# Kernel tuning notes

Measured on AMD Instinct MI355X. Metric: run time of the kernel, lower is better.

Reference implementation:

```python
import jax, jax.numpy as jnp
import numpy as np

EMBED_DIM = 1024
HEAD_SIZE = 128
B, S = 8, 2048

def setup_inputs() -> dict:
    rng = jax.random.key(0)
    k1, k2, k3, k4, k5, k6 = jax.random.split(rng, 6)
    std = 1.0 / EMBED_DIM  # nn.initializers.normal(stddev=1/embed_dim)
    return {
        "key": jax.random.normal(k1, (B, S, EMBED_DIM), dtype=jnp.float32),
        "query": jax.random.normal(k2, (B, S, EMBED_DIM), dtype=jnp.float32),
        "value": jax.random.normal(k3, (B, S, EMBED_DIM), dtype=jnp.float32),
        "W_Q": jax.random.normal(k4, (EMBED_DIM, HEAD_SIZE), dtype=jnp.float32) * std,
        "W_K": jax.random.normal(k5, (EMBED_DIM, HEAD_SIZE), dtype=jnp.float32) * std,
        "W_V": jax.random.normal(k6, (EMBED_DIM, HEAD_SIZE), dtype=jnp.float32) * std,
    }

def reference(key, query, value, W_Q, W_K, W_V):
    # Parallel retention: (Q K^T * causal_mask) V
    q_proj = query @ W_Q        # (B, S, H)
    k_proj = key @ W_K          # (B, S, H)
    v_proj = value @ W_V        # (B, S, H)
    ret = jnp.einsum("bsh,bth->bst", q_proj, k_proj)  # (B, S, S)
    # full_self_retention=False -> lower-triangular (causal) mask
    decay_matrix = jnp.tril(jnp.ones((S, S), dtype=ret.dtype))
    ret = ret * decay_matrix
    return ret @ v_proj          # (B, S, H)
```

## Files before the change

### kernel.cpp

```cpp
#include <hip/hip_runtime.h>
#include <cstdint>

#define B_  8
#define S_  2048
#define E_  1024
#define H_  128
#define NC_ 16

typedef __attribute__((ext_vector_type(8))) short bf16x8;
typedef __attribute__((ext_vector_type(4))) float f32x4;

__device__ __forceinline__ short f2bf(float f){
  uint32_t u = __builtin_bit_cast(uint32_t, f);
  u = (u + 0x7fffu + ((u >> 16) & 1u)) >> 16;
  return (short)u;
}
__device__ __forceinline__ float bf2f(short s){
  uint32_t u = ((uint32_t)(uint16_t)s) << 16;
  return __builtin_bit_cast(float, u);
}

__global__ __launch_bounds__(256) void wt_kernel(
    const float* __restrict__ WQ, const float* __restrict__ WK,
    const float* __restrict__ WV,
    short* __restrict__ WtQ, short* __restrict__ WtK, short* __restrict__ WtV)
{
  int which = blockIdx.z;
  const float* W = which == 0 ? WQ : which == 1 ? WK : WV;
  short* Wt      = which == 0 ? WtQ : which == 1 ? WtK : WtV;
  int k0 = blockIdx.x * 32, n0 = blockIdx.y * 32;
  __shared__ float t[32][33];
  int tx = threadIdx.x & 31, ty = threadIdx.x >> 5;
  #pragma unroll
  for (int i = 0; i < 4; i++)
    t[ty + i * 8][tx] = W[(size_t)(k0 + ty + i * 8) * H_ + n0 + tx];
  __syncthreads();
  #pragma unroll
  for (int i = 0; i < 4; i++)
    Wt[(size_t)(n0 + ty + i * 8) * E_ + k0 + tx] = f2bf(t[tx][ty + i * 8]);
}

__global__ __launch_bounds__(256) void proj_kernel(
    const float* __restrict__ Xq, const float* __restrict__ Xk,
    const float* __restrict__ Xv,
    const short* __restrict__ Wtq, const short* __restrict__ Wtk,
    const short* __restrict__ Wtv,
    short* __restrict__ q, short* __restrict__ k,
    short* __restrict__ kT, short* __restrict__ vT)
{
  int which = blockIdx.y;
  const float* X  = which == 0 ? Xq  : which == 1 ? Xk  : Xv;
  const short* Wt = which == 0 ? Wtq : which == 1 ? Wtk : Wtv;

  int tid = threadIdx.x, lane = tid & 63, wave = tid >> 6;
  int lr = lane & 15, lq = lane >> 4;
  int rowbase = blockIdx.x * 64 + wave * 16;

  __shared__ short Bs[128 * 136];

  const float* xr = X + (size_t)(rowbase + lr) * E_ + lq * 8;

  f32x4 acc[8];
  #pragma unroll
  for (int tn = 0; tn < 8; tn++) acc[tn] = (f32x4){0.f, 0.f, 0.f, 0.f};

  for (int kc = 0; kc < 8; kc++){
    if (kc) __syncthreads();
    #pragma unroll
    for (int v = 0; v < 8; v++){
      int c = v * 256 + tid;
      int n = c >> 4, off = (c & 15) * 8;
      *(bf16x8*)(&Bs[n * 136 + off]) =
          *(const bf16x8*)(Wt + (size_t)n * E_ + kc * 128 + off);
    }
    f32x4 ar[8];
    #pragma unroll
    for (int s = 0; s < 4; s++){
      ar[2 * s]     = *(const f32x4*)(xr + kc * 128 + s * 32);
      ar[2 * s + 1] = *(const f32x4*)(xr + kc * 128 + s * 32 + 4);
    }
    __syncthreads();
    #pragma unroll
    for (int s = 0; s < 4; s++){
      bf16x8 a;
      #pragma unroll
      for (int j = 0; j < 4; j++){
        a[j] = f2bf(ar[2 * s][j]); a[4 + j] = f2bf(ar[2 * s + 1][j]);
      }
      #pragma unroll
      for (int tn = 0; tn < 8; tn++){
        bf16x8 bfr = *(const bf16x8*)(&Bs[(tn * 16 + lr) * 136 + s * 32 + lq * 8]);
        acc[tn] = __builtin_amdgcn_mfma_f32_16x16x32_bf16(a, bfr, acc[tn], 0, 0, 0);
      }
    }
  }

  if (which <= 1){
    short* P = which == 0 ? q : k;
    #pragma unroll
    for (int tn = 0; tn < 8; tn++)
      #pragma unroll
      for (int r4 = 0; r4 < 4; r4++)
        P[(size_t)(rowbase + lq * 4 + r4) * H_ + tn * 16 + lr] = f2bf(acc[tn][r4]);
  }
  if (which >= 1){
    short* T = which == 1 ? kT : vT;
    int b = rowbase >> 11, srow = rowbase & 2047;
    #pragma unroll
    for (int tn = 0; tn < 8; tn++){
      union { short sh[4]; uint2 u; } pk;
      #pragma unroll
      for (int r4 = 0; r4 < 4; r4++) pk.sh[r4] = f2bf(acc[tn][r4]);
      *(uint2*)(T + ((size_t)b * H_ + tn * 16 + lr) * S_ + srow + lq * 4) = pk.u;
    }
  }
}

__global__ __launch_bounds__(256) void fused_state(
    const short* __restrict__ vT, const short* __restrict__ kT,
    short* __restrict__ Shi, short* __restrict__ Slo)
{
  int rh = blockIdx.x;
  int ch = blockIdx.y;
  int b  = blockIdx.z;
  int tid = threadIdx.x, lane = tid & 63, wave = tid >> 6;
  int lr = lane & 15, lq = lane >> 4;

  __shared__ short As[2][32 * 136];
  __shared__ short Bs[2][64 * 136];

  const short* vtb = vT + (size_t)b * H_ * S_ + (size_t)(rh * 32) * S_;
  const short* ktb = kT + (size_t)b * H_ * S_ + (size_t)(ch * 64) * S_;

  f32x4 acc[2];
  acc[0] = (f32x4){0.f, 0.f, 0.f, 0.f};
  acc[1] = (f32x4){0.f, 0.f, 0.f, 0.f};

  for (int j = 0; j < NC_; j++){
    size_t obase = (size_t)(b * NC_ + j) * 16384;
    #pragma unroll
    for (int tm = 0; tm < 2; tm++)
      #pragma unroll
      for (int r4 = 0; r4 < 4; r4++){
        int row = rh * 32 + tm * 16 + lq * 4 + r4;
        int col = ch * 64 + wave * 16 + lr;
        float v = acc[tm][r4];
        short h = f2bf(v);
        Shi[obase + (size_t)row * 128 + col] = h;
        Slo[obase + (size_t)row * 128 + col] = f2bf(v - bf2f(h));
      }
    if (j == NC_ - 1) break;

    int buf = j & 1;
    #pragma unroll
    for (int v = 0; v < 2; v++){
      int c = v * 256 + tid;
      int r = c >> 4, off = (c & 15) * 8;
      *(bf16x8*)(&As[buf][r * 136 + off]) =
          *(const bf16x8*)(vtb + (size_t)r * S_ + j * 128 + off);
    }
    #pragma unroll
    for (int v = 0; v < 4; v++){
      int c = v * 256 + tid;
      int r = c >> 4, off = (c & 15) * 8;
      *(bf16x8*)(&Bs[buf][r * 136 + off]) =
          *(const bf16x8*)(ktb + (size_t)r * S_ + j * 128 + off);
    }
    __syncthreads();

    #pragma unroll
    for (int s = 0; s < 4; s++){
      int t0 = s * 32;
      bf16x8 bfr = *(const bf16x8*)(&Bs[buf][(wave * 16 + lr) * 136 + t0 + lq * 8]);
      #pragma unroll
      for (int tm = 0; tm < 2; tm++){
        bf16x8 af = *(const bf16x8*)(&As[buf][(tm * 16 + lr) * 136 + t0 + lq * 8]);
        acc[tm] = __builtin_amdgcn_mfma_f32_16x16x32_bf16(af, bfr, acc[tm], 0, 0, 0);
      }
    }
  }
}

__global__ __launch_bounds__(256) void passC(
    const short* __restrict__ qb, const short* __restrict__ kb,
    const short* __restrict__ vT, const short* __restrict__ Shi,
    const short* __restrict__ Slo, float* __restrict__ out)
{
  int i = blockIdx.x, qtr = blockIdx.y, b = blockIdx.z;
  int roff = qtr * 32;
  int tid = threadIdx.x, lane = tid & 63, wave = tid >> 6;
  int wcol = wave * 32;
  int lr = lane & 15, lq = lane >> 4;

  __shared__ short Ss[32 * 136];
  __shared__ short Bt0[128 * 136];
  __shared__ short Bt1[128 * 136];

  const short* qbase = qb + ((size_t)b * S_ + i * 128 + roff) * H_;
  const short* kbase = kb + ((size_t)b * S_ + i * 128) * H_;
  const short* vtb   = vT + (size_t)b * H_ * S_ + i * 128;
  const short* shib  = Shi + (size_t)(b * NC_ + i) * 16384;
  const short* slob  = Slo + (size_t)(b * NC_ + i) * 16384;

  bf16x8 kst[8], vst[8], hst[8], lst[8];
  #pragma unroll
  for (int v = 0; v < 8; v++){
    int c = v * 256 + tid;
    int r = c >> 4, off = (c & 15) * 8;
    kst[v] = *(const bf16x8*)(kbase + (size_t)r * H_ + off);
    vst[v] = *(const bf16x8*)(vtb  + (size_t)r * S_ + off);
    hst[v] = *(const bf16x8*)(shib + (size_t)r * 128 + off);
    lst[v] = *(const bf16x8*)(slob + (size_t)r * 128 + off);
  }
  bf16x8 aq[2][4];
  #pragma unroll
  for (int tm = 0; tm < 2; tm++)
    #pragma unroll
    for (int hs = 0; hs < 4; hs++)
      aq[tm][hs] = *(const bf16x8*)(
          qbase + (size_t)(tm * 16 + lr) * H_ + hs * 32 + lq * 8);

  #pragma unroll
  for (int v = 0; v < 8; v++){
    int c = v * 256 + tid;
    int r = c >> 4, off = (c & 15) * 8;
    *(bf16x8*)(&Bt0[r * 136 + off]) = kst[v];
  }
  __syncthreads();

  f32x4 accS[2][2];
  #pragma unroll
  for (int a = 0; a < 2; a++)
    #pragma unroll
    for (int c = 0; c < 2; c++) accS[a][c] = (f32x4){0.f, 0.f, 0.f, 0.f};

  #pragma unroll
  for (int hs = 0; hs < 4; hs++){
    bf16x8 bf[2];
    #pragma unroll
    for (int tn = 0; tn < 2; tn++)
      bf[tn] = *(const bf16x8*)(&Bt0[(wcol + tn * 16 + lr) * 136 + hs * 32 + lq * 8]);
    #pragma unroll
    for (int tm = 0; tm < 2; tm++)
      #pragma unroll
      for (int tn = 0; tn < 2; tn++)
        accS[tm][tn] = __builtin_amdgcn_mfma_f32_16x16x32_bf16(
            aq[tm][hs], bf[tn], accS[tm][tn], 0, 0, 0);
  }

  #pragma unroll
  for (int tm = 0; tm < 2; tm++)
    #pragma unroll
    for (int tn = 0; tn < 2; tn++)
      #pragma unroll
      for (int r4 = 0; r4 < 4; r4++){
        int row = tm * 16 + lq * 4 + r4;
        int col = wcol + tn * 16 + lr;
        float vv = (col <= roff + row) ? accS[tm][tn][r4] : 0.f;
        Ss[row * 136 + col] = f2bf(vv);
      }
  #pragma unroll
  for (int v = 0; v < 8; v++){
    int c = v * 256 + tid;
    int r = c >> 4, off = (c & 15) * 8;
    *(bf16x8*)(&Bt1[r * 136 + off]) = vst[v];
  }
  f32x4 acc[2][2];
  #pragma unroll
  for (int a = 0; a < 2; a++)
    #pragma unroll
    for (int c = 0; c < 2; c++) acc[a][c] = (f32x4){0.f, 0.f, 0.f, 0.f};
  __syncthreads();

  #pragma unroll
  for (int s = 0; s < 4; s++){
    int t0 = s * 32;
    bf16x8 af[2], bf[2];
    #pragma unroll
    for (int tm = 0; tm < 2; tm++)
      af[tm] = *(const bf16x8*)(&Ss[(tm * 16 + lr) * 136 + t0 + lq * 8]);
    #pragma unroll
    for (int tn = 0; tn < 2; tn++)
      bf[tn] = *(const bf16x8*)(&Bt1[(wcol + tn * 16 + lr) * 136 + t0 + lq * 8]);
    #pragma unroll
    for (int tm = 0; tm < 2; tm++)
      #pragma unroll
      for (int tn = 0; tn < 2; tn++)
        acc[tm][tn] = __builtin_amdgcn_mfma_f32_16x16x32_bf16(
            af[tm], bf[tn], acc[tm][tn], 0, 0, 0);
  }
  #pragma unroll
  for (int v = 0; v < 8; v++){
    int c = v * 256 + tid;
    int r = c >> 4, off = (c & 15) * 8;
    *(bf16x8*)(&Bt0[r * 136 + off]) = hst[v];
  }
  __syncthreads();

  #pragma unroll
  for (int hs = 0; hs < 4; hs++){
    bf16x8 bf[2];
    #pragma unroll
    for (int tn = 0; tn < 2; tn++)
      bf[tn] = *(const bf16x8*)(&Bt0[(wcol + tn * 16 + lr) * 136 + hs * 32 + lq * 8]);
    #pragma unroll
    for (int tm = 0; tm < 2; tm++)
      #pragma unroll
      for (int tn = 0; tn < 2; tn++)
        acc[tm][tn] = __builtin_amdgcn_mfma_f32_16x16x32_bf16(
            aq[tm][hs], bf[tn], acc[tm][tn], 0, 0, 0);
  }
  #pragma unroll
  for (int v = 0; v < 8; v++){
    int c = v * 256 + tid;
    int r = c >> 4, off = (c & 15) * 8;
    *(bf16x8*)(&Bt1[r * 136 + off]) = lst[v];
  }
  __syncthreads();

  #pragma unroll
  for (int hs = 0; hs < 4; hs++){
    bf16x8 bf[2];
    #pragma unroll
    for (int tn = 0; tn < 2; tn++)
      bf[tn] = *(const bf16x8*)(&Bt1[(wcol + tn * 16 + lr) * 136 + hs * 32 + lq * 8]);
    #pragma unroll
    for (int tm = 0; tm < 2; tm++)
      #pragma unroll
      for (int tn = 0; tn < 2; tn++)
        acc[tm][tn] = __builtin_amdgcn_mfma_f32_16x16x32_bf16(
            aq[tm][hs], bf[tn], acc[tm][tn], 0, 0, 0);
  }

  float* ob = out + ((size_t)b * S_ + i * 128 + roff) * H_;
  #pragma unroll
  for (int tm = 0; tm < 2; tm++)
    #pragma unroll
    for (int tn = 0; tn < 2; tn++)
      #pragma unroll
      for (int r4 = 0; r4 < 4; r4++){
        int row = tm * 16 + lq * 4 + r4;
        int col = wcol + tn * 16 + lr;
        ob[(size_t)row * H_ + col] = acc[tm][tn][r4];
      }
}

extern "C" void kernel_launch(void* const* d_in, const int* in_sizes, int n_in,
                              void* d_out, int out_size, void* d_ws, size_t ws_size,
                              hipStream_t stream) {
  const float* key   = (const float*)d_in[0];
  const float* query = (const float*)d_in[1];
  const float* value = (const float*)d_in[2];
  const float* WQ    = (const float*)d_in[3];
  const float* WK    = (const float*)d_in[4];
  const float* WV    = (const float*)d_in[5];
  float* out = (float*)d_out;

  char* w = (char*)d_ws;
  short* WtQ = (short*)(w + 0);
  short* WtK = (short*)(w + 262144);
  short* WtV = (short*)(w + 524288);
  size_t o = 786432;
  short* q  = (short*)(w + o); o += 4194304;
  short* k  = (short*)(w + o); o += 4194304;
  short* kT = (short*)(w + o); o += 4194304;
  short* vT = (short*)(w + o); o += 4194304;
  short* Shi= (short*)(w + o); o += 4194304;
  short* Slo= (short*)(w + o); o += 4194304;

  wt_kernel   <<<dim3(32, 4, 3),       256, 0, stream>>>(WQ, WK, WV, WtQ, WtK, WtV);
  proj_kernel <<<dim3(256, 3),         256, 0, stream>>>(query, key, value,
                                                         WtQ, WtK, WtV, q, k, kT, vT);
  fused_state <<<dim3(4, 2, B_),       256, 0, stream>>>(vT, kT, Shi, Slo);
  passC       <<<dim3(NC_, 4, B_),     256, 0, stream>>>(q, k, vT, Shi, Slo, out);
}
```

Before: 237.5 us.

## Double-buffer projection kernel K-loop with register prefetch of next chunk

Restructures the projection GEMM K-loop into 64-wide chunks with two LDS buffers. The next chunk's weights and activations are prefetched into registers while the current chunk is computed, and each iteration ends with a single waitcnt+barrier. This is meant to hide global-load latency behind the MFMA work and remove the second barrier per chunk. In exchange it uses more registers, and the hand-written barrier sequencing adds risk.

Result: slower. 260.4 us (+9.6%).

```diff
diff --git a/kernel.cpp b/kernel.cpp
--- a/kernel.cpp
+++ b/kernel.cpp
@@ -56,7 +56,7 @@
   int lr = lane & 15, lq = lane >> 4;
   int rowbase = blockIdx.x * 64 + wave * 16;
 
-  __shared__ short Bs[128 * 136];
+  __shared__ short Bs[2][128 * 72];
 
   const float* xr = X + (size_t)(rowbase + lr) * E_ + lq * 8;
 
@@ -64,24 +64,35 @@
   #pragma unroll
   for (int tn = 0; tn < 8; tn++) acc[tn] = (f32x4){0.f, 0.f, 0.f, 0.f};
 
-  for (int kc = 0; kc < 8; kc++){
-    if (kc) __syncthreads();
-    #pragma unroll
-    for (int v = 0; v < 8; v++){
+  bf16x8 brA[4], brB[4];
+  f32x4 a0[4], a1[4];
+
+  auto BLOAD = [&](bf16x8* br, int t){
+    #pragma unroll
+    for (int v = 0; v < 4; v++){
       int c = v * 256 + tid;
-      int n = c >> 4, off = (c & 15) * 8;
-      *(bf16x8*)(&Bs[n * 136 + off]) =
-          *(const bf16x8*)(Wt + (size_t)n * E_ + kc * 128 + off);
-    }
-    f32x4 ar[8];
-    #pragma unroll
-    for (int s = 0; s < 4; s++){
-      ar[2 * s]     = *(const f32x4*)(xr + kc * 128 + s * 32);
-      ar[2 * s + 1] = *(const f32x4*)(xr + kc * 128 + s * 32 + 4);
-    }
-    __syncthreads();
-    #pragma unroll
-    for (int s = 0; s < 4; s++){
+      int n = c >> 3, off = (c & 7) * 8;
+      br[v] = *(const bf16x8*)(Wt + (size_t)n * E_ + t * 64 + off);
+    }
+  };
+  auto BCOMMIT = [&](int buf, const bf16x8* br){
+    #pragma unroll
+    for (int v = 0; v < 4; v++){
+      int c = v * 256 + tid;
+      int n = c >> 3, off = (c & 7) * 8;
+      *(bf16x8*)(&Bs[buf][n * 72 + off]) = br[v];
+    }
+  };
+  auto LOADA = [&](f32x4* a, int t){
+    #pragma unroll
+    for (int s = 0; s < 2; s++){
+      a[2 * s]     = *(const f32x4*)(xr + t * 64 + s * 32);
+      a[2 * s + 1] = *(const f32x4*)(xr + t * 64 + s * 32 + 4);
+    }
+  };
+  auto COMPUTE = [&](int buf, const f32x4* ar){
+    #pragma unroll
+    for (int s = 0; s < 2; s++){
       bf16x8 a;
       #pragma unroll
       for (int j = 0; j < 4; j++){
@@ -89,11 +100,34 @@
       }
       #pragma unroll
       for (int tn = 0; tn < 8; tn++){
-        bf16x8 bfr = *(const bf16x8*)(&Bs[(tn * 16 + lr) * 136 + s * 32 + lq * 8]);
+        bf16x8 bfr = *(const bf16x8*)(&Bs[buf][(tn * 16 + lr) * 72 + s * 32 + lq * 8]);
         acc[tn] = __builtin_amdgcn_mfma_f32_16x16x32_bf16(a, bfr, acc[tn], 0, 0, 0);
       }
     }
-  }
+  };
+  #define SYNC_LDS() do { asm volatile("s_waitcnt lgkmcnt(0)" ::: "memory"); \
+                          __builtin_amdgcn_s_barrier(); } while (0)
+
+  BLOAD(brA, 0); LOADA(a0, 0);
+  BCOMMIT(0, brA);
+  SYNC_LDS();
+
+  for (int p = 0; p < 8; p++){
+    int te = 2 * p;
+    BLOAD(brB, te + 1); LOADA(a1, te + 1);
+    COMPUTE(0, a0);
+    BCOMMIT(1, brB);
+    SYNC_LDS();
+    if (p < 7){
+      BLOAD(brA, te + 2); LOADA(a0, te + 2);
+      COMPUTE(1, a1);
+      BCOMMIT(0, brA);
+      SYNC_LDS();
+    } else {
+      COMPUTE(1, a1);
+    }
+  }
+  #undef SYNC_LDS
 
   if (which <= 1){
     short* P = which == 0 ? q : k;
```
